# Optimization experiments

Hardware: AMD Instinct MI355X
Metric: run time of the kernel (lower is better)

Reference implementation:

```python
import jax, jax.numpy as jnp
import numpy as np

N, E, D, H = 100000, 800000, 128, 4
DK = D // H
SCALE = 1.0 / np.sqrt(D)  # keep logits tame with random weights
EPS = 1e-5


def _layernorm(x, g, b):
    mu = jnp.mean(x, axis=-1, keepdims=True)
    var = jnp.mean(jnp.square(x - mu), axis=-1, keepdims=True)
    return (x - mu) * jax.lax.rsqrt(var + EPS) * g + b


def setup_inputs() -> dict:
    key = jax.random.key(0)
    ks = jax.random.split(key, 14)
    inp = {
        'h': jax.random.normal(ks[0], (N, D), jnp.float32),
        'e_ij': jax.random.normal(ks[1], (E, D), jnp.float32),
        'W1': jax.random.normal(ks[2], (D, D), jnp.float32) * SCALE,
        'W2': jax.random.normal(ks[3], (D, D), jnp.float32) * SCALE,
        'W3': jax.random.normal(ks[4], (D, D), jnp.float32) * SCALE,
        'W4': jax.random.normal(ks[5], (D, D), jnp.float32) * SCALE,
        'W5': jax.random.normal(ks[6], (D, D), jnp.float32) * SCALE,
        'W6': jax.random.normal(ks[7], (D, D), jnp.float32) * SCALE,
        'ln_gamma': jnp.ones((D,), jnp.float32),
        'ln_beta': jnp.zeros((D,), jnp.float32),
        'mlp_w1': jax.random.normal(ks[8], (D, 2 * D), jnp.float32) * SCALE,
        'mlp_w2': jax.random.normal(ks[9], (2 * D, D), jnp.float32) * (1.0 / np.sqrt(2 * D)),
        'src': jax.random.randint(ks[10], (E,), 0, N, jnp.int32),
        'dst': jax.random.randint(ks[11], (E,), 0, N, jnp.int32),
    }
    return inp


def reference(h, e_ij, W1, W2, W3, W4, W5, W6, ln_gamma, ln_beta, mlp_w1, mlp_w2, src, dst):
    u = (h @ W1).reshape(N, H, DK)      # src-side query
    v = (h @ W2).reshape(N, H, DK)      # dst-side
    x3 = (e_ij @ W3).reshape(E, H, DK)
    # m = v[dst] + x_ij ; attn = u[src] * m (elementwise per head/channel)
    m = v[dst] + x3                      # [E,H,DK]
    attn = (u[src] * m) / np.sqrt(DK)    # [E,H,DK]
    # edge_softmax: segment softmax over incoming edges of each dst node
    amax = jax.ops.segment_max(attn, dst, num_segments=N)   # [N,H,DK]
    ex = jnp.exp(attn - amax[dst])
    denom = jax.ops.segment_sum(ex, dst, num_segments=N)    # [N,H,DK]
    alpha = ex / denom[dst]
    k = (h @ W4).reshape(N, H, DK)
    x5 = (e_ij @ W5).reshape(E, H, DK)
    m2 = k[dst] + x5                     # [E,H,DK]
    agg = jax.ops.segment_sum(alpha * m2, dst, num_segments=N).reshape(N, D)
    h1 = h @ W6 + agg
    h1 = _layernorm(h1, ln_gamma, ln_beta)
    mlp_out = jax.nn.relu(h1 @ mlp_w1) @ mlp_w2
    h2 = _layernorm(h1 + mlp_out, ln_gamma, ln_beta)  # same LayerNorm params reused
    return h2
```

## Files before the change

kernel.cpp:

```cpp
#include <hip/hip_runtime.h>
#include <hip/hip_bf16.h>

#define N_NODES 100000
#define N_EDGES 800000

typedef __attribute__((ext_vector_type(8))) short short8v;
typedef __attribute__((ext_vector_type(4))) float f32x4;

__device__ __forceinline__ unsigned short f2bf(float f) {
    __hip_bfloat16 b = __float2bfloat16(f);
    return *(unsigned short*)&b;
}
__device__ __forceinline__ float bf2f(unsigned short u) {
    return __uint_as_float((unsigned)u << 16);
}
__device__ __forceinline__ unsigned pack2(float lo, float hi) {
    return (unsigned)f2bf(lo) | ((unsigned)f2bf(hi) << 16);
}

__device__ __forceinline__ void gload_lds16(const void* g, void* l) {
    __builtin_amdgcn_global_load_lds(
        (const __attribute__((address_space(1))) unsigned int*)g,
        (__attribute__((address_space(3))) unsigned int*)l,
        16, 0, 0);
}

__device__ __forceinline__ int xcd_swizzle(int orig, int q, int r) {
    int xcd = orig & 7, loc = orig >> 3;
    return (xcd < r ? xcd * (q + 1) : r * (q + 1) + (xcd - r) * q) + loc;
}

__global__ __launch_bounds__(256) void hist_dst(
    const int* __restrict__ dst, int* __restrict__ counts)
{
    int e = blockIdx.x * 256 + threadIdx.x;
    if (e < N_EDGES) atomicAdd(&counts[dst[e]], 1);
}

__global__ __launch_bounds__(256) void scan_p1(
    const int* __restrict__ in, int* __restrict__ partials, int n)
{
    __shared__ int ws[4];
    int t = threadIdx.x, lane = t & 63, wv = t >> 6;
    int base = blockIdx.x * 1024;
    int s = 0;
#pragma unroll
    for (int i = 0; i < 4; ++i) {
        int idx = base + i * 256 + t;
        s += (idx < n) ? in[idx] : 0;
    }
#pragma unroll
    for (int off = 1; off < 64; off <<= 1) s += __shfl_xor(s, off);
    if (lane == 0) ws[wv] = s;
    __syncthreads();
    if (t == 0) partials[blockIdx.x] = ws[0] + ws[1] + ws[2] + ws[3];
}

__global__ __launch_bounds__(64) void scan_p2(
    int* __restrict__ partials, int nb, int* __restrict__ total_out)
{
    int lane = threadIdx.x;
    int carry = 0;
    for (int base = 0; base < nb; base += 64) {
        int idx = base + lane;
        int v = (idx < nb) ? partials[idx] : 0;
        int s = v;
#pragma unroll
        for (int off = 1; off < 64; off <<= 1) {
            int w = __shfl_up(s, off);
            if (lane >= off) s += w;
        }
        if (idx < nb) partials[idx] = s - v + carry;
        carry += __shfl(s, 63);
    }
    if (lane == 0) *total_out = carry;
}

__global__ __launch_bounds__(256) void scan_p3(
    const int* __restrict__ in, int* __restrict__ out, int* __restrict__ cursor,
    const int* __restrict__ partials, int n)
{
    __shared__ int ws[4];
    __shared__ int wpre[4];
    __shared__ int s_tot;
    int t = threadIdx.x, lane = t & 63, wv = t >> 6;
    int base = blockIdx.x * 1024;
    int carry = partials[blockIdx.x];
    for (int sub = 0; sub < 4; ++sub) {
        int idx = base + sub * 256 + t;
        int v = (idx < n) ? in[idx] : 0;
        int s = v;
#pragma unroll
        for (int off = 1; off < 64; off <<= 1) {
            int w = __shfl_up(s, off);
            if (lane >= off) s += w;
        }
        if (lane == 63) ws[wv] = s;
        __syncthreads();
        if (t == 0) {
            int a = 0;
#pragma unroll
            for (int i = 0; i < 4; ++i) { wpre[i] = a; a += ws[i]; }
            s_tot = a;
        }
        __syncthreads();
        int excl = s - v + wpre[wv] + carry;
        if (idx < n) { out[idx] = excl; if (cursor) cursor[idx] = excl; }
        carry += s_tot;
        __syncthreads();
    }
}

__global__ __launch_bounds__(256) void scatter_edges(
    const int* __restrict__ dst, const int* __restrict__ src,
    int* __restrict__ cursor,
    int* __restrict__ edge_ord, int* __restrict__ src_ord,
    int* __restrict__ dst_ord)
{
    int e = blockIdx.x * 256 + threadIdx.x;
    if (e < N_EDGES) {
        int d = dst[e];
        int pos = atomicAdd(&cursor[d], 1);
        edge_ord[pos] = e;
        src_ord[pos] = src[e];
        dst_ord[pos] = d;
    }
}

__global__ __launch_bounds__(256) void calc_npieces(
    const int* __restrict__ offsets, int* __restrict__ npieces)
{
    int n = blockIdx.x * 256 + threadIdx.x;
    if (n < N_NODES) {
        int b = offsets[n], e = offsets[n + 1];
        npieces[n] = (e > b) ? (((e - 1) >> 6) - (b >> 6) + 1) : 0;
    }
}

__global__ __launch_bounds__(256) void prep_weights(
    const float* __restrict__ W1, const float* __restrict__ W2,
    const float* __restrict__ W3, const float* __restrict__ W4,
    const float* __restrict__ W5, const float* __restrict__ W6,
    const float* __restrict__ mw1, const float* __restrict__ mw2,
    unsigned short* __restrict__ w3t, unsigned short* __restrict__ w5t,
    unsigned short* __restrict__ wcatt,
    unsigned short* __restrict__ mw1t, unsigned short* __restrict__ mw2t)
{
    int bid = blockIdx.x;
    if (bid < 64) {
        int t = bid * 256 + threadIdx.x;
        int r = t >> 7, c = t & 127;
        w3t[c * 128 + r] = f2bf(W3[t]);
        w5t[c * 128 + r] = f2bf(W5[t]);
    } else if (bid < 320) {
        int t = (bid - 64) * 256 + threadIdx.x;
        int n = t >> 7, k = t & 127;
        const float* Wm = (n < 128) ? W1 : (n < 256) ? W2 : (n < 384) ? W4 : W6;
        wcatt[t] = f2bf(Wm[k * 128 + (n & 127)]);
    } else {
        int t = (bid - 320) * 256 + threadIdx.x;
        if (t < 32768) {
            int n = t >> 7, k = t & 127;
            mw1t[t] = f2bf(mw1[k * 256 + n]);
        } else {
            int s = t - 32768;
            int n = s >> 8, k = s & 255;
            mw2t[s] = f2bf(mw2[k * 128 + n]);
        }
    }
}

__global__ __launch_bounds__(256) void gemm_node(
    const float* __restrict__ A, const unsigned short* __restrict__ Bt,
    unsigned short* __restrict__ uvkb, float* __restrict__ hw6f)
{
    const int t = threadIdx.x;
    const int lane = t & 63, wv = t >> 6;
    const int l15 = lane & 15, kg = lane >> 4;
    const int m0 = blockIdx.x * 64;
    const int n0 = blockIdx.y * 128;
    const int M = N_NODES, K = 128;

    int arow = m0 + wv * 16 + l15;
    int arow_c = arow < M ? arow : M - 1;
    const float* ap = A + (size_t)arow_c * K + kg * 8;

    f32x4 acc[8];
#pragma unroll
    for (int nt = 0; nt < 8; ++nt) acc[nt] = (f32x4){0.f, 0.f, 0.f, 0.f};

    for (int ko = 0; ko < K; ko += 32) {
        float4 f0 = *(const float4*)(ap + ko);
        float4 f1 = *(const float4*)(ap + ko + 4);
        short8v af;
        af[0] = (short)f2bf(f0.x); af[1] = (short)f2bf(f0.y);
        af[2] = (short)f2bf(f0.z); af[3] = (short)f2bf(f0.w);
        af[4] = (short)f2bf(f1.x); af[5] = (short)f2bf(f1.y);
        af[6] = (short)f2bf(f1.z); af[7] = (short)f2bf(f1.w);
#pragma unroll
        for (int nt = 0; nt < 8; ++nt) {
            short8v bf = *(const short8v*)(Bt + (size_t)(n0 + nt * 16 + l15) * K + ko + kg * 8);
            acc[nt] = __builtin_amdgcn_mfma_f32_16x16x32_bf16(af, bf, acc[nt], 0, 0, 0);
        }
    }
#pragma unroll
    for (int nt = 0; nt < 8; ++nt) {
#pragma unroll
        for (int r = 0; r < 4; ++r) {
            int row = m0 + wv * 16 + kg * 4 + r;
            if (row < M) {
                int col = n0 + nt * 16 + l15;
                float vfl = acc[nt][r];
                if (n0 < 384) uvkb[(size_t)row * 384 + col] = f2bf(vfl);
                else          hw6f[(size_t)row * 128 + col - 384] = vfl;
            }
        }
    }
}

__global__ __launch_bounds__(256, 4) void edge_agg(
    const float* __restrict__ e_ij,
    const unsigned short* __restrict__ w3t, const unsigned short* __restrict__ w5t,
    const unsigned short* __restrict__ uvkb,
    const int* __restrict__ edge_ord, const int* __restrict__ src_ord,
    const int* __restrict__ dst_ord,
    const int* __restrict__ offsets, const int* __restrict__ ppos,
    float* __restrict__ dpart, float* __restrict__ apart)
{
    __shared__ __align__(16) float e_s[64 * 128];
    __shared__ int s_eid[64], s_src[64], s_dst[64];
    __shared__ int s_sb[64], s_se[64], s_pi[64];
    __shared__ int s_nseg;

    const int t  = threadIdx.x;
    const int lane = t & 63, wv = t >> 6;
    const int l15 = lane & 15, kg = lane >> 4;
    const int cb = wv * 32 + 2 * l15;
    const float inv = 0.17677669529663687f;

    const int nwg = N_EDGES / 64;
    const int bswz = xcd_swizzle((int)blockIdx.x, nwg >> 3, nwg & 7);
    const int e0 = bswz * 64;

    if (t < 64) {
        s_eid[t] = edge_ord[e0 + t];
        s_src[t] = src_ord[e0 + t];
        int d = dst_ord[e0 + t];
        s_dst[t] = d;
        int dprev = __shfl_up(d, 1);
        bool bnd = (t == 0) || (d != dprev);
        unsigned long long mask = __ballot(bnd);
        int sid = __popcll(mask & ((1ull << t) - 1ull));
        if (bnd) {
            s_sb[sid] = t;
            s_pi[sid] = ppos[d] + bswz - (offsets[d] >> 6);
            if (t > 0) s_se[sid - 1] = t;
        }
        if (t == 63) {
            int ns = __popcll(mask);
            s_se[ns - 1] = 64;
            s_nseg = ns;
        }
    }
    __syncthreads();

#pragma unroll
    for (int i = 0; i < 8; ++i) {
        int c = i * 256 + t;
        int row = c >> 5, j = c & 31;
        int js = j ^ (row & 7);
        const float* g = e_ij + (size_t)s_eid[row] * 128 + js * 4;
        void* l = (void*)((char*)(&e_s[0]) + (size_t)i * 4096 + (size_t)wv * 1024);
        gload_lds16(g, l);
    }
    __syncthreads();

    unsigned short* eb = (unsigned short*)&e_s[0];
    {
        const int crow = t >> 2, q = t & 3;
        float4 fr[8];
#pragma unroll
        for (int i = 0; i < 8; ++i) {
            int j = (q * 8 + i) ^ (crow & 7);
            fr[i] = *(const float4*)(&e_s[crow * 128 + j * 4]);
        }
        __syncthreads();
#pragma unroll
        for (int i = 0; i < 4; ++i) {
            short8v pk;
            pk[0] = (short)f2bf(fr[2 * i].x);     pk[1] = (short)f2bf(fr[2 * i].y);
            pk[2] = (short)f2bf(fr[2 * i].z);     pk[3] = (short)f2bf(fr[2 * i].w);
            pk[4] = (short)f2bf(fr[2 * i + 1].x); pk[5] = (short)f2bf(fr[2 * i + 1].y);
            pk[6] = (short)f2bf(fr[2 * i + 1].z); pk[7] = (short)f2bf(fr[2 * i + 1].w);
            int c = (q * 4 + i) ^ (crow & 15);
            *(short8v*)(eb + crow * 128 + c * 8) = pk;
        }
    }
    __syncthreads();

    const int nseg = __builtin_amdgcn_readfirstlane(s_nseg);

    f32x4 a3[4][2], a5[4][2];
#pragma unroll
    for (int m = 0; m < 4; ++m) {
        a3[m][0] = (f32x4){0.f, 0.f, 0.f, 0.f};
        a3[m][1] = (f32x4){0.f, 0.f, 0.f, 0.f};
        a5[m][0] = (f32x4){0.f, 0.f, 0.f, 0.f};
        a5[m][1] = (f32x4){0.f, 0.f, 0.f, 0.f};
    }
    {
        const unsigned short* b3p0 = w3t + (size_t)(cb + 0) * 128 + kg * 8;
        const unsigned short* b3p1 = w3t + (size_t)(cb + 1) * 128 + kg * 8;
        const unsigned short* b5p0 = w5t + (size_t)(cb + 0) * 128 + kg * 8;
        const unsigned short* b5p1 = w5t + (size_t)(cb + 1) * 128 + kg * 8;
#pragma unroll
        for (int kidx = 0; kidx < 4; ++kidx) {
            const int ko = kidx * 32;
            short8v b30 = *(const short8v*)(b3p0 + ko);
            short8v b31 = *(const short8v*)(b3p1 + ko);
            short8v b50 = *(const short8v*)(b5p0 + ko);
            short8v b51 = *(const short8v*)(b5p1 + ko);
#pragma unroll
            for (int m = 0; m < 4; ++m) {
                const int row = m * 16 + l15;
                short8v af = *(const short8v*)(eb + row * 128 + (((kidx << 2) | kg) ^ l15) * 8);
                a3[m][0] = __builtin_amdgcn_mfma_f32_16x16x32_bf16(af, b30, a3[m][0], 0, 0, 0);
                a3[m][1] = __builtin_amdgcn_mfma_f32_16x16x32_bf16(af, b31, a3[m][1], 0, 0, 0);
                a5[m][0] = __builtin_amdgcn_mfma_f32_16x16x32_bf16(af, b50, a5[m][0], 0, 0, 0);
                a5[m][1] = __builtin_amdgcn_mfma_f32_16x16x32_bf16(af, b51, a5[m][1], 0, 0, 0);
            }
        }
    }

#pragma unroll
    for (int m = 0; m < 4; ++m) {
#pragma unroll
        for (int r = 0; r < 4; ++r) {
            int le = m * 16 + kg * 4 + r;
            int d  = s_dst[le];
            int sv = s_src[le];
            unsigned upk = *(const unsigned*)&uvkb[(size_t)sv * 384 + cb];
            unsigned vpk = *(const unsigned*)&uvkb[(size_t)d * 384 + 128 + cb];
            float u0 = bf2f((unsigned short)(upk & 0xffffu));
            float u1 = bf2f((unsigned short)(upk >> 16));
            float v0 = bf2f((unsigned short)(vpk & 0xffffu));
            float v1 = bf2f((unsigned short)(vpk >> 16));
            float at0 = u0 * (v0 + a3[m][0][r]) * inv;
            float at1 = u1 * (v1 + a3[m][1][r]) * inv;
            float ex0 = __expf(fminf(at0, 80.f));
            float ex1 = __expf(fminf(at1, 80.f));
            a3[m][0][r] = ex0;
            a3[m][1][r] = ex1;
            a5[m][0][r] = ex0 * a5[m][0][r];
            a5[m][1][r] = ex1 * a5[m][1][r];
        }
    }

    for (int sg = 0; sg < nseg; ++sg) {
        const int b  = __builtin_amdgcn_readfirstlane(s_sb[sg]);
        const int e2 = __builtin_amdgcn_readfirstlane(s_se[sg]);
        const int pi = __builtin_amdgcn_readfirstlane(s_pi[sg]);
        float d0 = 0.f, d1 = 0.f, g0 = 0.f, g1 = 0.f;
#pragma unroll
        for (int m = 0; m < 4; ++m) {
            if (b < m * 16 + 16 && e2 > m * 16) {
#pragma unroll
                for (int r = 0; r < 4; ++r) {
                    int slot = m * 16 + kg * 4 + r;
                    bool in = (slot >= b) && (slot < e2);
                    d0 += in ? a3[m][0][r] : 0.f;
                    d1 += in ? a3[m][1][r] : 0.f;
                    g0 += in ? a5[m][0][r] : 0.f;
                    g1 += in ? a5[m][1][r] : 0.f;
                }
            }
        }
        d0 += __shfl_xor(d0, 16); d0 += __shfl_xor(d0, 32);
        d1 += __shfl_xor(d1, 16); d1 += __shfl_xor(d1, 32);
        g0 += __shfl_xor(g0, 16); g0 += __shfl_xor(g0, 32);
        g1 += __shfl_xor(g1, 16); g1 += __shfl_xor(g1, 32);
        if (kg == 0) {
            *(float2*)&dpart[(size_t)pi * 128 + cb] = make_float2(d0, d1);
            *(float2*)&apart[(size_t)pi * 128 + cb] = make_float2(g0, g1);
        }
    }
}

__global__ __launch_bounds__(256) void node_finalize(
    const float* __restrict__ hw6f, const unsigned short* __restrict__ uvkb,
    const float* __restrict__ dpart, const float* __restrict__ apart,
    const int* __restrict__ ppos,
    const float* __restrict__ gamma, const float* __restrict__ beta,
    float* __restrict__ h1, unsigned short* __restrict__ h1b)
{
    int n = blockIdx.x * 4 + (threadIdx.x >> 6);
    int lane = threadIdx.x & 63;
    int p0 = ppos[n], p1 = ppos[n + 1];
    float de0 = 0.f, de1 = 0.f, g0 = 0.f, g1 = 0.f;
    for (int j = p0; j < p1; ++j) {
        float2 dv = *(const float2*)&dpart[(size_t)j * 128 + lane * 2];
        float2 av = *(const float2*)&apart[(size_t)j * 128 + lane * 2];
        de0 += dv.x; de1 += dv.y;
        g0  += av.x; g1  += av.y;
    }
    unsigned kpk = *(const unsigned*)&uvkb[(size_t)n * 384 + 256 + lane * 2];
    float k0 = bf2f((unsigned short)(kpk & 0xffffu));
    float k1 = bf2f((unsigned short)(kpk >> 16));
    float2 hw = *(const float2*)&hw6f[(size_t)n * 128 + lane * 2];
    float x0 = hw.x + (de0 > 0.f ? k0 + g0 / de0 : 0.f);
    float x1 = hw.y + (de1 > 0.f ? k1 + g1 / de1 : 0.f);
    float s = x0 + x1;
#pragma unroll
    for (int off = 1; off < 64; off <<= 1) s += __shfl_xor(s, off);
    float mu = s * (1.f / 128.f);
    float d0 = x0 - mu, d1 = x1 - mu;
    float ss = d0 * d0 + d1 * d1;
#pragma unroll
    for (int off = 1; off < 64; off <<= 1) ss += __shfl_xor(ss, off);
    float rs = rsqrtf(ss * (1.f / 128.f) + 1e-5f);
    float2 g = *(const float2*)&gamma[lane * 2];
    float2 b = *(const float2*)&beta[lane * 2];
    float o0 = d0 * rs * g.x + b.x;
    float o1 = d1 * rs * g.y + b.y;
    size_t base = (size_t)n * 128 + lane * 2;
    *(float2*)&h1[base] = make_float2(o0, o1);
    *(unsigned*)&h1b[base] = pack2(o0, o1);
}

__global__ __launch_bounds__(256, 4) void mlp_tail(
    const unsigned short* __restrict__ A,
    const float* __restrict__ res,
    const unsigned short* __restrict__ mw1t, const unsigned short* __restrict__ mw2t,
    const float* __restrict__ gamma, const float* __restrict__ beta,
    float* __restrict__ out)
{
    __shared__ __align__(16) unsigned short hid[64 * 264];

    const int t = threadIdx.x;
    const int lane = t & 63, wv = t >> 6;
    const int l15 = lane & 15, kg = lane >> 4;
    const int m0 = blockIdx.x * 64;
    const int M = N_NODES;

    {
        int arow = m0 + wv * 16 + l15;
        int arow_c = arow < M ? arow : M - 1;
        const unsigned short* ap = A + (size_t)arow_c * 128 + kg * 8;
        f32x4 acc[16];
#pragma unroll
        for (int nt = 0; nt < 16; ++nt) acc[nt] = (f32x4){0.f, 0.f, 0.f, 0.f};
#pragma unroll
        for (int kidx = 0; kidx < 4; ++kidx) {
            const int ko = kidx * 32;
            short8v af = *(const short8v*)(ap + ko);
#pragma unroll
            for (int nt = 0; nt < 16; ++nt) {
                short8v bf = *(const short8v*)(mw1t + (size_t)(nt * 16 + l15) * 128 + ko + kg * 8);
                acc[nt] = __builtin_amdgcn_mfma_f32_16x16x32_bf16(af, bf, acc[nt], 0, 0, 0);
            }
        }
#pragma unroll
        for (int nt = 0; nt < 16; ++nt) {
#pragma unroll
            for (int r = 0; r < 4; ++r) {
                int row = wv * 16 + kg * 4 + r;
                int col = nt * 16 + l15;
                hid[row * 264 + col] = f2bf(fmaxf(acc[nt][r], 0.f));
            }
        }
    }
    __syncthreads();

    {
        const int lrow = wv * 16 + l15;
        f32x4 acc[8];
#pragma unroll
        for (int nt = 0; nt < 8; ++nt) acc[nt] = (f32x4){0.f, 0.f, 0.f, 0.f};
#pragma unroll
        for (int kidx = 0; kidx < 8; ++kidx) {
            const int ko = kidx * 32;
            short8v af = *(const short8v*)&hid[lrow * 264 + ko + kg * 8];
#pragma unroll
            for (int nt = 0; nt < 8; ++nt) {
                short8v bf = *(const short8v*)(mw2t + (size_t)(nt * 16 + l15) * 256 + ko + kg * 8);
                acc[nt] = __builtin_amdgcn_mfma_f32_16x16x32_bf16(af, bf, acc[nt], 0, 0, 0);
            }
        }
        float gv[8], bv[8];
#pragma unroll
        for (int nt = 0; nt < 8; ++nt) {
            gv[nt] = gamma[nt * 16 + l15];
            bv[nt] = beta[nt * 16 + l15];
        }
#pragma unroll
        for (int r = 0; r < 4; ++r) {
            int row = m0 + wv * 16 + kg * 4 + r;
            int rc = row < M ? row : M - 1;
            float x[8];
            float s = 0.f;
#pragma unroll
            for (int nt = 0; nt < 8; ++nt) {
                x[nt] = acc[nt][r] + res[(size_t)rc * 128 + nt * 16 + l15];
                s += x[nt];
            }
#pragma unroll
            for (int off = 1; off < 16; off <<= 1) s += __shfl_xor(s, off);
            float mu = s * (1.f / 128.f);
            float ss = 0.f;
#pragma unroll
            for (int nt = 0; nt < 8; ++nt) {
                float d = x[nt] - mu;
                ss += d * d;
            }
#pragma unroll
            for (int off = 1; off < 16; off <<= 1) ss += __shfl_xor(ss, off);
            float rsv = rsqrtf(ss * (1.f / 128.f) + 1e-5f);
            if (row < M) {
#pragma unroll
                for (int nt = 0; nt < 8; ++nt)
                    out[(size_t)row * 128 + nt * 16 + l15] =
                        (x[nt] - mu) * rsv * gv[nt] + bv[nt];
            }
        }
    }
}

extern "C" void kernel_launch(void* const* d_in, const int* in_sizes, int n_in,
                              void* d_out, int out_size, void* d_ws, size_t ws_size,
                              hipStream_t stream)
{
    const float* h    = (const float*)d_in[0];
    const float* e_ij = (const float*)d_in[1];
    const float* W1   = (const float*)d_in[2];
    const float* W2   = (const float*)d_in[3];
    const float* W3   = (const float*)d_in[4];
    const float* W4   = (const float*)d_in[5];
    const float* W5   = (const float*)d_in[6];
    const float* W6   = (const float*)d_in[7];
    const float* ln_g = (const float*)d_in[8];
    const float* ln_b = (const float*)d_in[9];
    const float* mw1  = (const float*)d_in[10];
    const float* mw2  = (const float*)d_in[11];
    const int*   src  = (const int*)d_in[12];
    const int*   dst  = (const int*)d_in[13];
    float* out = (float*)d_out;

    float* ws = (float*)d_ws;
    float* hw6f  = ws;
    float* h1    = ws + 12800000;
    float* dpart = ws + 25600000;
    float* apart = ws + 40100000;
    unsigned short* uvkb  = (unsigned short*)(ws + 54600000);
    unsigned short* h1b   = (unsigned short*)(ws + 73800000);
    unsigned short* w3t   = (unsigned short*)(ws + 93000000);
    unsigned short* w5t   = w3t + 16384;
    unsigned short* wcatt = w5t + 16384;
    unsigned short* mw1t  = wcatt + 65536;
    unsigned short* mw2t  = mw1t + 32768;
    int* ibase    = (int*)(ws + 93100000);
    int* counts   = ibase;
    int* offsets  = ibase + 100000;
    int* cursor   = ibase + 200001;
    int* npieces  = ibase + 300001;
    int* ppos     = ibase + 400001;
    int* partials = ibase + 500102;
    int* edge_ord = ibase + 500230;
    int* src_ord  = edge_ord + N_EDGES;
    int* dst_ord  = src_ord + N_EDGES;

    dim3 blk(256);
    hipMemsetAsync(counts, 0, N_NODES * sizeof(int), stream);

    hist_dst<<<N_EDGES / 256, blk, 0, stream>>>(dst, counts);
    scan_p1<<<98, blk, 0, stream>>>(counts, partials, N_NODES);
    scan_p2<<<1, 64, 0, stream>>>(partials, 98, offsets + N_NODES);
    scan_p3<<<98, blk, 0, stream>>>(counts, offsets, cursor, partials, N_NODES);
    scatter_edges<<<N_EDGES / 256, blk, 0, stream>>>(dst, src, cursor,
                                                     edge_ord, src_ord, dst_ord);
    calc_npieces<<<391, blk, 0, stream>>>(offsets, npieces);
    scan_p1<<<98, blk, 0, stream>>>(npieces, partials, N_NODES);
    scan_p2<<<1, 64, 0, stream>>>(partials, 98, ppos + N_NODES);
    scan_p3<<<98, blk, 0, stream>>>(npieces, ppos, (int*)nullptr, partials, N_NODES);

    prep_weights<<<576, blk, 0, stream>>>(W1, W2, W3, W4, W5, W6, mw1, mw2,
                                          w3t, w5t, wcatt, mw1t, mw2t);

    gemm_node<<<dim3(1563, 4), blk, 0, stream>>>(h, wcatt, uvkb, hw6f);

    edge_agg<<<N_EDGES / 64, blk, 0, stream>>>(e_ij, w3t, w5t, uvkb,
                                               edge_ord, src_ord, dst_ord,
                                               offsets, ppos, dpart, apart);

    node_finalize<<<N_NODES / 4, blk, 0, stream>>>(hw6f, uvkb, dpart, apart, ppos,
                                                   ln_g, ln_b, h1, h1b);

    mlp_tail<<<1563, blk, 0, stream>>>(h1b, h1, mw1t, mw2t, ln_g, ln_b, out);
}
```

Before: 612.7 us.

## Stage A tile once in LDS as bf16 and loop over all four N panels

The node GEMM used to launch four column-panel blocks per 64-row tile, and each one reloaded and reconverted the same fp32 rows of h. Now one block loads the 64x128 fp32 tile into swizzled LDS with direct global-to-LDS loads, converts it to bf16 in place, and reuses it for all four output panels. The aim is to cut redundant reads of h and the repeated conversions. In exchange each block does four times the work with fewer blocks, uses 32KB of LDS, and adds barriers.

```diff
diff --git a/kernel.cpp b/kernel.cpp
--- a/kernel.cpp
+++ b/kernel.cpp
@@ -170,49 +170,80 @@
     }
 }
 
-__global__ __launch_bounds__(256) void gemm_node(
+__global__ __launch_bounds__(256, 4) void gemm_node(
     const float* __restrict__ A, const unsigned short* __restrict__ Bt,
     unsigned short* __restrict__ uvkb, float* __restrict__ hw6f)
 {
+    __shared__ __align__(16) float a_s[64 * 128];
+
     const int t = threadIdx.x;
     const int lane = t & 63, wv = t >> 6;
     const int l15 = lane & 15, kg = lane >> 4;
     const int m0 = blockIdx.x * 64;
-    const int n0 = blockIdx.y * 128;
-    const int M = N_NODES, K = 128;
-
-    int arow = m0 + wv * 16 + l15;
-    int arow_c = arow < M ? arow : M - 1;
-    const float* ap = A + (size_t)arow_c * K + kg * 8;
-
-    f32x4 acc[8];
-#pragma unroll
-    for (int nt = 0; nt < 8; ++nt) acc[nt] = (f32x4){0.f, 0.f, 0.f, 0.f};
-
-    for (int ko = 0; ko < K; ko += 32) {
-        float4 f0 = *(const float4*)(ap + ko);
-        float4 f1 = *(const float4*)(ap + ko + 4);
-        short8v af;
-        af[0] = (short)f2bf(f0.x); af[1] = (short)f2bf(f0.y);
-        af[2] = (short)f2bf(f0.z); af[3] = (short)f2bf(f0.w);
-        af[4] = (short)f2bf(f1.x); af[5] = (short)f2bf(f1.y);
-        af[6] = (short)f2bf(f1.z); af[7] = (short)f2bf(f1.w);
+    const int M = N_NODES;
+
+#pragma unroll
+    for (int i = 0; i < 8; ++i) {
+        int c = i * 256 + t;
+        int row = c >> 5, j = c & 31;
+        int js = j ^ (row & 7);
+        int gr = m0 + row; if (gr >= M) gr = M - 1;
+        const float* g = A + (size_t)gr * 128 + js * 4;
+        void* l = (void*)((char*)(&a_s[0]) + (size_t)i * 4096 + (size_t)wv * 1024);
+        gload_lds16(g, l);
+    }
+    __syncthreads();
+
+    unsigned short* ab = (unsigned short*)&a_s[0];
+    {
+        const int crow = t >> 2, q = t & 3;
+        float4 fr[8];
+#pragma unroll
+        for (int i = 0; i < 8; ++i) {
+            int j = (q * 8 + i) ^ (crow & 7);
+            fr[i] = *(const float4*)(&a_s[crow * 128 + j * 4]);
+        }
+        __syncthreads();
+#pragma unroll
+        for (int i = 0; i < 4; ++i) {
+            short8v pk;
+            pk[0] = (short)f2bf(fr[2 * i].x);     pk[1] = (short)f2bf(fr[2 * i].y);
+            pk[2] = (short)f2bf(fr[2 * i].z);     pk[3] = (short)f2bf(fr[2 * i].w);
+            pk[4] = (short)f2bf(fr[2 * i + 1].x); pk[5] = (short)f2bf(fr[2 * i + 1].y);
+            pk[6] = (short)f2bf(fr[2 * i + 1].z); pk[7] = (short)f2bf(fr[2 * i + 1].w);
+            int c = (q * 4 + i) ^ (crow & 15);
+            *(short8v*)(ab + crow * 128 + c * 8) = pk;
+        }
+    }
+    __syncthreads();
+
+    for (int panel = 0; panel < 4; ++panel) {
+        const int n0 = panel * 128;
+        f32x4 acc[8];
+#pragma unroll
+        for (int nt = 0; nt < 8; ++nt) acc[nt] = (f32x4){0.f, 0.f, 0.f, 0.f};
+#pragma unroll
+        for (int kidx = 0; kidx < 4; ++kidx) {
+            const int ko = kidx * 32;
+            const int row = wv * 16 + l15;
+            short8v af = *(const short8v*)(ab + row * 128 + (((kidx << 2) | kg) ^ l15) * 8);
+#pragma unroll
+            for (int nt = 0; nt < 8; ++nt) {
+                short8v bf = *(const short8v*)(Bt + (size_t)(n0 + nt * 16 + l15) * 128 + ko + kg * 8);
+                acc[nt] = __builtin_amdgcn_mfma_f32_16x16x32_bf16(af, bf, acc[nt], 0, 0, 0);
+            }
+        }
 #pragma unroll
         for (int nt = 0; nt < 8; ++nt) {
-            short8v bf = *(const short8v*)(Bt + (size_t)(n0 + nt * 16 + l15) * K + ko + kg * 8);
-            acc[nt] = __builtin_amdgcn_mfma_f32_16x16x32_bf16(af, bf, acc[nt], 0, 0, 0);
-        }
-    }
-#pragma unroll
-    for (int nt = 0; nt < 8; ++nt) {
-#pragma unroll
-        for (int r = 0; r < 4; ++r) {
-            int row = m0 + wv * 16 + kg * 4 + r;
-            if (row < M) {
-                int col = n0 + nt * 16 + l15;
-                float vfl = acc[nt][r];
-                if (n0 < 384) uvkb[(size_t)row * 384 + col] = f2bf(vfl);
-                else          hw6f[(size_t)row * 128 + col - 384] = vfl;
+#pragma unroll
+            for (int r = 0; r < 4; ++r) {
+                int row = m0 + wv * 16 + kg * 4 + r;
+                if (row < M) {
+                    int col = n0 + nt * 16 + l15;
+                    float vfl = acc[nt][r];
+                    if (panel < 3) uvkb[(size_t)row * 384 + col] = f2bf(vfl);
+                    else           hw6f[(size_t)row * 128 + col - 384] = vfl;
+                }
             }
         }
     }
@@ -585,7 +616,7 @@
     prep_weights<<<576, blk, 0, stream>>>(W1, W2, W3, W4, W5, W6, mw1, mw2,
                                           w3t, w5t, wcatt, mw1t, mw2t);
 
-    gemm_node<<<dim3(1563, 4), blk, 0, stream>>>(h, wcatt, uvkb, hw6f);
+    gemm_node<<<1563, blk, 0, stream>>>(h, wcatt, uvkb, hw6f);
 
     edge_agg<<<N_EDGES / 64, blk, 0, stream>>>(e_ij, w3t, w5t, uvkb,
                                                edge_ord, src_ord, dst_ord,
```

After: 607.3 us. About the same (-0.9%).
